# Performance work log

Hardware: AMD Instinct MI355X
Metric: run time of the kernel (lower is better)

The kernel has to match this reference:

```python
import jax, jax.numpy as jnp
import numpy as np

B, S, F, H, A = 256, 128, 512, 1024, 18


def setup_inputs() -> dict:
    key = jax.random.key(0)
    ks = jax.random.split(key, 16)
    u = lambda k, shape, fan: jax.random.uniform(k, shape, jnp.float32, -1.0, 1.0) / np.sqrt(fan)
    return {
        "obs": jax.random.normal(ks[0], (B, S, F), jnp.float32),
        "hx": jax.random.normal(ks[1], (B, H), jnp.float32),
        "cx": jax.random.normal(ks[2], (B, H), jnp.float32),
        "behaviour_acts": jax.random.randint(ks[3], (B, S, 1), 0, A),
        "W1": u(ks[4], (H, F), F), "b1": u(ks[5], (H,), F),
        "W_ih": u(ks[6], (4 * H, H), H), "b_ih": u(ks[7], (4 * H,), H),
        "W_hh": u(ks[8], (4 * H, H), H), "b_hh": u(ks[9], (4 * H,), H),
        "W_v": u(ks[10], (1, H), H), "b_v": u(ks[11], (1,), H),
        "W_l": u(ks[12], (A, H), H), "b_l": u(ks[13], (A,), H),
    }


def reference(obs, hx, cx, behaviour_acts, W1, b1, W_ih, b_ih, W_hh, b_hh, W_v, b_v, W_l, b_l):
    # MLP body: [B,S,F] -> [B,S,H]
    x = jax.nn.relu(jnp.einsum("bsf,hf->bsh", obs, W1) + b1)
    # precompute input-to-gate projection for all timesteps (one big GEMM)
    xg = jnp.einsum("bsh,gh->bsg", x, W_ih) + b_ih  # [B,S,4H]

    def step(carry, xg_t):
        h, c = carry
        gates = xg_t + h @ W_hh.T + b_hh  # [B,4H], gate order i,f,g,o (torch LSTMCell)
        i, f, g, o = jnp.split(gates, 4, axis=-1)
        c = jax.nn.sigmoid(f) * c + jax.nn.sigmoid(i) * jnp.tanh(g)
        h = jax.nn.sigmoid(o) * jnp.tanh(c)
        return (h, c), h

    _, hs = jax.lax.scan(step, (hx, cx), jnp.swapaxes(xg, 0, 1))
    output = jnp.swapaxes(hs, 0, 1)  # [B,S,H]

    value = output @ W_v.T + b_v  # [B,S,1]
    logits = output @ W_l.T + b_l  # [B,S,A]
    # torch Categorical(probs=softmax(logits)) => log-prob via log_softmax
    logp = jax.nn.log_softmax(logits, axis=-1)
    acts = behaviour_acts.reshape(logits.shape[0], logits.shape[1], 1)
    log_probs = jnp.take_along_axis(logp, acts, axis=-1)  # [B,S,1]
    entropy = -jnp.sum(jnp.exp(logp) * logp, axis=-1, keepdims=True)  # [B,S,1]
    return log_probs, entropy, value
```

## Files before the change

### kernel.cpp

```cpp
#include <hip/hip_runtime.h>

#define B_ 256
#define S_ 128
#define SP1 (S_+1)
#define F_ 512
#define H_ 1024
#define A_ 18
#define M_ (B_*S_)
#define G_ (4*H_)
#define CH_ 16
#define CR_ (B_*CH_)

typedef unsigned short u16;
typedef __attribute__((ext_vector_type(8))) _Float16 f16x8;
typedef __attribute__((ext_vector_type(4))) _Float16 f16x4;
typedef __attribute__((ext_vector_type(8))) short   s16x8;
typedef __attribute__((ext_vector_type(4))) float f32x4;
typedef __attribute__((ext_vector_type(4))) unsigned int u32x4;

__device__ __forceinline__ float bf2f(u16 u){
  union{unsigned int i; float f;} v; v.i=((unsigned int)u)<<16; return v.f;
}
__device__ __forceinline__ u16 f2bf(float f){
  unsigned int i=__float_as_uint(f);
  unsigned int r=(i+0x7fffu+((i>>16)&1u))>>16;
  return (u16)r;
}
__device__ __forceinline__ u16 f2h(float f){
  _Float16 h=(_Float16)f;
  union{_Float16 h; u16 u;} v; v.h=h; return v.u;
}
__device__ __forceinline__ float ldf(const void* p, size_t i, int m){
  return m ? ((const float*)p)[i] : bf2f(((const u16*)p)[i]);
}
__device__ __forceinline__ f16x8 load8_h(const void* base, size_t off, int m){
  f16x8 v;
  if(m==2) return *(const f16x8*)((const u16*)base + off);
  if(m==1){
    const float* f=(const float*)base + off;
    float4 a=*(const float4*)f; float4 b=*(const float4*)(f+4);
    v[0]=(_Float16)a.x; v[1]=(_Float16)a.y; v[2]=(_Float16)a.z; v[3]=(_Float16)a.w;
    v[4]=(_Float16)b.x; v[5]=(_Float16)b.y; v[6]=(_Float16)b.z; v[7]=(_Float16)b.w;
    return v;
  }
  s16x8 w=*(const s16x8*)((const u16*)base + off);
#pragma unroll
  for(int k=0;k<8;k++) v[k]=(_Float16)bf2f((u16)w[k]);
  return v;
}

__device__ __forceinline__ u32x4 load_c16(const void* p){
  u32x4 r;
  asm volatile("global_load_dwordx4 %0, %1, off sc0 sc1" : "=v"(r) : "v"(p));
  return r;
}
__device__ __forceinline__ void store_c2(u16* p, u16 v){
  unsigned int vv=v;
  asm volatile("global_store_short %0, %1, off sc0 sc1" :: "v"(p), "v"(vv) : "memory");
}
__device__ __forceinline__ int load_c4(const int* p){
  int r;
  asm volatile("global_load_dword %0, %1, off sc0 sc1" : "=v"(r) : "v"(p));
  return r;
}
__device__ __forceinline__ void store_c4(int* p, int v){
  asm volatile("global_store_dword %0, %1, off sc0 sc1" :: "v"(p), "v"(v) : "memory");
}

__device__ __forceinline__ void bar_flags32(int* flags, int target, int gi, int lane, int w){
  asm volatile("s_waitcnt vmcnt(0)" ::: "memory");
  __syncthreads();
  if(w==0){
    if(lane==0) store_c4(flags+gi, target);
    while(true){
      int v=load_c4(flags+(lane&31));
      asm volatile("s_waitcnt vmcnt(0)" ::: "memory");
      if(__all(v>=target)) break;
      __builtin_amdgcn_s_sleep(1);
    }
  }
  __syncthreads();
}

template<int ROWS, int MAP>
__device__ __forceinline__ void stage(const void* base, int mode, int lda, int k0,
                                      int rowoff, int t0, u16* lds, int tid){
  if(mode==2){
    constexpr int NI=(ROWS*8)/256;
    int wv=tid>>6, l=tid&63;
#pragma unroll
    for(int i=0;i<NI;i++){
      int s0=i*256+(wv<<6), s=s0+l;
      int r=s>>3, gc=(s&7)^(r&7);
      int p=rowoff+r, sr;
      if(MAP==0)      sr=p;
      else if(MAP==1) sr=(p&3)*H_+(p>>2);
      else            sr=(p>>4)*S_+t0+(p&15);
      const u16* src=(const u16*)base + (size_t)sr*lda + k0 + gc*8;
      u16* dst=lds + s0*8;
      __builtin_amdgcn_global_load_lds((const __attribute__((address_space(1))) unsigned int*)src,
                                       (__attribute__((address_space(3))) unsigned int*)dst,
                                       16, 0, 0);
    }
  } else {
#pragma unroll
    for(int s0=tid; s0<ROWS*8; s0+=256){
      int r=s0>>3, gc=s0&7, lc=gc^(r&7);
      int p=rowoff+r, sr;
      if(MAP==0)      sr=p;
      else if(MAP==1) sr=(p&3)*H_+(p>>2);
      else            sr=(p>>4)*S_+t0+(p&15);
      f16x8 v=load8_h(base, (size_t)sr*lda + k0 + gc*8, mode);
      *(f16x8*)(lds + r*64 + lc*8)=v;
    }
  }
}

__device__ __forceinline__ f16x8 frag_ld(const u16* lds, int r0, int kc, int lane){
  int r = r0 + (lane&15);
  int c = (kc + (lane>>4)) ^ (r&7);
  return *(const f16x8*)(lds + r*64 + c*8);
}

template<int AMAP, int BMAP, int OUTMODE>
__global__ __launch_bounds__(256,3) void gemm128(const void* A, const void* Bt, void* C,
    const float* __restrict__ biasf, const int* __restrict__ flag,
    int K, int lda, int ldb, int ldc, int t0, int amode, int bmode){
  int m=*flag;
  int am = amode<0 ? m : amode;
  int bm_ = bmode<0 ? m : bmode;
  __shared__ u16 As[128*64];
  __shared__ u16 Bs[128*64];
  int tid=threadIdx.x, lane=tid&63, w=tid>>6;
  int bm=blockIdx.y*128, bn=blockIdx.x*128;
  int wm=(w&1)*64, wn=(w>>1)*64;
  f32x4 acc[4][4];
#pragma unroll
  for(int i=0;i<4;i++)
#pragma unroll
    for(int j=0;j<4;j++) acc[i][j]=(f32x4)(0.f);
  for(int k0=0;k0<K;k0+=64){
    stage<128,AMAP>(A , am,  lda, k0, bm, t0, As, tid);
    stage<128,BMAP>(Bt, bm_, ldb, k0, bn, t0, Bs, tid);
    __syncthreads();
#pragma unroll
    for(int kk=0;kk<2;kk++){
      f16x8 af[4], bq[4];
#pragma unroll
      for(int i=0;i<4;i++) af[i]=frag_ld(As, wm+i*16, kk*4, lane);
#pragma unroll
      for(int j=0;j<4;j++) bq[j]=frag_ld(Bs, wn+j*16, kk*4, lane);
#pragma unroll
      for(int i=0;i<4;i++)
#pragma unroll
        for(int j=0;j<4;j++)
          acc[i][j]=__builtin_amdgcn_mfma_f32_16x16x32_f16(af[i],bq[j],acc[i][j],0,0,0);
    }
    __syncthreads();
  }
  int rl=lane>>4, cl=lane&15;
#pragma unroll
  for(int j=0;j<4;j++){
    int col=bn+wn+j*16+cl;
    float bb=biasf[col];
#pragma unroll
    for(int i=0;i<4;i++){
#pragma unroll
      for(int r=0;r<4;r++){
        int row=bm+wm+i*16+rl*4+r;
        float v=acc[i][j][r]+bb;
        if(OUTMODE==0){ v=fmaxf(v,0.f); ((u16*)C)[(size_t)row*ldc+col]=f2h(v); }
        else if(OUTMODE==2){ ((u16*)C)[(size_t)row*ldc+col]=f2h(v); }
        else { ((float*)C)[(size_t)row*ldc+col]=v; }
      }
    }
  }
}

__global__ __launch_bounds__(512,2) void lstm_persist(u16* __restrict__ hh,
        const u16* __restrict__ Whhp, const u16* __restrict__ xgp,
        float* __restrict__ cst, int* __restrict__ cntc, int tbase){
  __shared__ u16 As[16*2048];
  __shared__ float gs[32*132];
  int tid=threadIdx.x, lane=tid&63, w=tid>>6;
  int grp=blockIdx.x&7, ci=blockIdx.x>>3;
  int bm=grp*32, bn=ci*128;
  int* flags = cntc + grp*64;

  f16x8 bw[32];
#pragma unroll
  for(int t=0;t<32;t++){
    int p = bn + w*16 + (lane&15);
    int k = t*32 + (lane>>4)*8;
    bw[t]=*(const f16x8*)(Whhp + (size_t)p*H_ + k);
  }
#pragma unroll
  for(int t=0;t<32;t++) asm volatile("" : "+a"(bw[t]));

  int rl0=tid>>5, rl1=(tid+512)>>5, u0=tid&31;
  int gu=(bn>>2)+u0;
  float c0=cst[(size_t)(bm+rl0)*H_+gu];
  float c1=cst[(size_t)(bm+rl1)*H_+gu];

  for(int dt=0;dt<CH_;dt++){
    f16x4 xv0=*(const f16x4*)(xgp + ((size_t)(bm+rl0)*CH_+dt)*G_ + bn + u0*4);
    f16x4 xv1=*(const f16x4*)(xgp + ((size_t)(bm+rl1)*CH_+dt)*G_ + bn + u0*4);
    if(dt) bar_flags32(flags, tbase+dt, ci, lane, w);
    const u16* hbase = hh + (size_t)(tbase+dt)*H_;
    {
      u32x4 tmp[4];
#pragma unroll
      for(int i=0;i<4;i++){
        int s=tid+i*512, kt=s>>8, r=(s>>3)&31, gc=s&7;
        tmp[i]=*(const u32x4*)(hbase + (size_t)(bm+r)*(SP1*H_) + kt*64 + gc*8);
      }
#pragma unroll
      for(int i=0;i<4;i++){
        int s=tid+i*512, kt=s>>8, r=(s>>3)&31, gc=s&7, lc=gc^(r&7);
        *(u32x4*)(As + kt*2048 + r*64 + lc*8)=tmp[i];
      }
    }
    __syncthreads();
    u32x4 tmp2[4];
#pragma unroll
    for(int i=0;i<4;i++){
      int s=tid+(i+4)*512, kt=s>>8, r=(s>>3)&31, gc=s&7;
      tmp2[i]=*(const u32x4*)(hbase + (size_t)(bm+r)*(SP1*H_) + kt*64 + gc*8);
    }
    f32x4 acc0=(f32x4)(0.f), acc1=(f32x4)(0.f);
#pragma unroll
    for(int t=0;t<16;t++){
      int kt=t>>1, kk=t&1;
      f16x8 af0=frag_ld(As+kt*2048, 0,  kk*4, lane);
      f16x8 af1=frag_ld(As+kt*2048, 16, kk*4, lane);
      acc0=__builtin_amdgcn_mfma_f32_16x16x32_f16(af0,bw[t],acc0,0,0,0);
      acc1=__builtin_amdgcn_mfma_f32_16x16x32_f16(af1,bw[t],acc1,0,0,0);
    }
#pragma unroll
    for(int i=0;i<4;i++){
      int s=tid+(i+4)*512, kt=s>>8, r=(s>>3)&31, gc=s&7, lc=gc^(r&7);
      *(u32x4*)(As + kt*2048 + r*64 + lc*8)=tmp2[i];
    }
    __syncthreads();
#pragma unroll
    for(int t=16;t<32;t++){
      int kt=t>>1, kk=t&1;
      f16x8 af0=frag_ld(As+kt*2048, 0,  kk*4, lane);
      f16x8 af1=frag_ld(As+kt*2048, 16, kk*4, lane);
      acc0=__builtin_amdgcn_mfma_f32_16x16x32_f16(af0,bw[t],acc0,0,0,0);
      acc1=__builtin_amdgcn_mfma_f32_16x16x32_f16(af1,bw[t],acc1,0,0,0);
    }
#pragma unroll
    for(int r=0;r<4;r++){
      gs[(   (lane>>4)*4+r)*132 + w*16+(lane&15)]=acc0[r];
      gs[(16+(lane>>4)*4+r)*132 + w*16+(lane&15)]=acc1[r];
    }
    __syncthreads();
    {
      float4 gv=*(const float4*)&gs[rl0*132+u0*4];
      float ii=1.f/(1.f+__expf(-(gv.x+(float)xv0[0])));
      float ff=1.f/(1.f+__expf(-(gv.y+(float)xv0[1])));
      float gg=1.f-2.f/(__expf(2.f*(gv.z+(float)xv0[2]))+1.f);
      float oo=1.f/(1.f+__expf(-(gv.w+(float)xv0[3])));
      c0=ff*c0+ii*gg;
      float th=1.f-2.f/(__expf(2.f*c0)+1.f);
      store_c2(hh + ((size_t)(bm+rl0)*SP1 + tbase+dt+1)*H_ + gu, f2h(oo*th));
    }
    {
      float4 gv=*(const float4*)&gs[rl1*132+u0*4];
      float ii=1.f/(1.f+__expf(-(gv.x+(float)xv1[0])));
      float ff=1.f/(1.f+__expf(-(gv.y+(float)xv1[1])));
      float gg=1.f-2.f/(__expf(2.f*(gv.z+(float)xv1[2]))+1.f);
      float oo=1.f/(1.f+__expf(-(gv.w+(float)xv1[3])));
      c1=ff*c1+ii*gg;
      float th=1.f-2.f/(__expf(2.f*c1)+1.f);
      store_c2(hh + ((size_t)(bm+rl1)*SP1 + tbase+dt+1)*H_ + gu, f2h(oo*th));
    }
  }
  cst[(size_t)(bm+rl0)*H_+gu]=c0;
  cst[(size_t)(bm+rl1)*H_+gu]=c1;
}

__global__ __launch_bounds__(256,2) void lstm_step(u16* __restrict__ hh, int slotAbs, int dt,
        const void* __restrict__ Whh, const u16* __restrict__ xg,
        float* __restrict__ cst, const int* __restrict__ flag){
  int m=*flag;
  __shared__ u16 As[64*64];
  __shared__ u16 Bs[64*64];
  __shared__ float gs[64*64];
  int tid=threadIdx.x, lane=tid&63, w=tid>>6;
  int bm=blockIdx.y*64, bn=blockIdx.x*64;
  int wm=(w&1)*32, wn=(w>>1)*32;
  f32x4 acc[2][2];
#pragma unroll
  for(int i=0;i<2;i++)
#pragma unroll
    for(int j=0;j<2;j++) acc[i][j]=(f32x4)(0.f);
  for(int k0=0;k0<H_;k0+=64){
    stage<64,0>(hh + (size_t)slotAbs*H_, 2, SP1*H_, k0, bm, 0, As, tid);
    stage<64,1>(Whh,                     m, H_,     k0, bn, 0, Bs, tid);
    __syncthreads();
#pragma unroll
    for(int kk=0;kk<2;kk++){
      f16x8 af[2], bq[2];
#pragma unroll
      for(int i=0;i<2;i++) af[i]=frag_ld(As, wm+i*16, kk*4, lane);
#pragma unroll
      for(int j=0;j<2;j++) bq[j]=frag_ld(Bs, wn+j*16, kk*4, lane);
#pragma unroll
      for(int i=0;i<2;i++)
#pragma unroll
        for(int j=0;j<2;j++)
          acc[i][j]=__builtin_amdgcn_mfma_f32_16x16x32_f16(af[i],bq[j],acc[i][j],0,0,0);
    }
    __syncthreads();
  }
  int rl=lane>>4, cl=lane&15;
#pragma unroll
  for(int j=0;j<2;j++){
    int coll=wn+j*16+cl;
#pragma unroll
    for(int i=0;i<2;i++){
#pragma unroll
      for(int r=0;r<4;r++){
        int rowl=wm+i*16+rl*4+r;
        float xv=(float)((const _Float16*)xg)[((size_t)(bm+rowl)*CH_+dt)*G_ + bn+coll];
        gs[rowl*64+coll]=acc[i][j][r] + xv;
      }
    }
  }
  __syncthreads();
#pragma unroll
  for(int p=0;p<4;p++){
    int idx=p*256+tid;
    int rowl=idx>>4, u=idx&15;
    float4 gv = *(const float4*)&gs[rowl*64+u*4];
    float ii=1.f/(1.f+__expf(-gv.x));
    float ff=1.f/(1.f+__expf(-gv.y));
    float gg=1.f-2.f/(__expf(2.f*gv.z)+1.f);
    float oo=1.f/(1.f+__expf(-gv.w));
    int gb=bm+rowl;
    int gu=(bn>>2)+u;
    size_t ci=(size_t)gb*H_+gu;
    float cn=ff*cst[ci]+ii*gg;
    cst[ci]=cn;
    float th=1.f-2.f/(__expf(2.f*cn)+1.f);
    hh[((size_t)gb*SP1 + slotAbs+1)*H_ + gu]=f2h(oo*th);
  }
}

__global__ __launch_bounds__(256,2) void heads_full(const u16* __restrict__ hh,
      const void* __restrict__ Wl, const void* __restrict__ Wv,
      const float* __restrict__ blf, const int* __restrict__ acts,
      void* __restrict__ out, const int* __restrict__ flag){
  int m=*flag;
  int rg = blockIdx.x*4 + (threadIdx.x>>6);
  int lane = threadIdx.x & 63;
  int b=rg>>7, t=rg&(S_-1);
  const u16* h = hh + ((size_t)b*SP1 + t+1)*H_;
  u32x4 hv0=load_c16(h + lane*16);
  u32x4 hv1=load_c16(h + lane*16 + 8);
  f16x8 h0=__builtin_bit_cast(f16x8,hv0), h1=__builtin_bit_cast(f16x8,hv1);
  float hv[16];
#pragma unroll
  for(int k=0;k<8;k++){ hv[k]=(float)h0[k]; hv[8+k]=(float)h1[k]; }
  float dots[19];
#pragma unroll
  for(int j=0;j<19;j++){
    const void* wrow = (j<18) ? Wl : Wv;
    size_t roff = (j<18) ? (size_t)j*H_ : 0;
    float wv_[16];
    if(m){
      const float* f=(const float*)wrow + roff + lane*16;
      float4 a=*(const float4*)f, b2=*(const float4*)(f+4), c=*(const float4*)(f+8), d=*(const float4*)(f+12);
      wv_[0]=a.x;wv_[1]=a.y;wv_[2]=a.z;wv_[3]=a.w; wv_[4]=b2.x;wv_[5]=b2.y;wv_[6]=b2.z;wv_[7]=b2.w;
      wv_[8]=c.x;wv_[9]=c.y;wv_[10]=c.z;wv_[11]=c.w; wv_[12]=d.x;wv_[13]=d.y;wv_[14]=d.z;wv_[15]=d.w;
    } else {
      const u16* ub=(const u16*)wrow + roff + lane*16;
      s16x8 w0=*(const s16x8*)ub, w1=*(const s16x8*)(ub+8);
#pragma unroll
      for(int k=0;k<8;k++){ wv_[k]=bf2f((u16)w0[k]); wv_[8+k]=bf2f((u16)w1[k]); }
    }
    float d=0.f;
#pragma unroll
    for(int k=0;k<16;k++) d += hv[k]*wv_[k];
#pragma unroll
    for(int mm=1;mm<64;mm<<=1) d += __shfl_xor(d, mm, 64);
    dots[j]=d;
  }
  float lg[18];
#pragma unroll
  for(int j=0;j<18;j++) lg[j]=dots[j]+blf[j];
  float value=dots[18]+blf[18];
  float mx=lg[0];
#pragma unroll
  for(int j=1;j<18;j++) mx=fmaxf(mx,lg[j]);
  float se=0.f, s1=0.f;
#pragma unroll
  for(int j=0;j<18;j++){ float e=__expf(lg[j]-mx); se+=e; s1+=e*(lg[j]-mx); }
  float lse=__logf(se);
  int a=acts[rg];
  float la=0.f;
#pragma unroll
  for(int j=0;j<18;j++) la = (j==a) ? lg[j] : la;
  float lp=la-mx-lse;
  float ent=lse - s1/se;
  if(lane==0){
    if(m){
      ((float*)out)[rg]=lp; ((float*)out)[M_+rg]=ent; ((float*)out)[2*M_+rg]=value;
    } else {
      ((u16*)out)[rg]=f2bf(lp); ((u16*)out)[M_+rg]=f2bf(ent); ((u16*)out)[2*M_+rg]=f2bf(value);
    }
  }
}

__global__ void detect(const u16* __restrict__ obs_w, int* __restrict__ flag){
  __shared__ float red[256];
  float mx=0.f;
  for(int i=threadIdx.x;i<4096;i+=256) mx=fmaxf(mx,fabsf(bf2f(obs_w[i])));
  red[threadIdx.x]=mx; __syncthreads();
  for(int s=128;s>0;s>>=1){
    if(threadIdx.x<s) red[threadIdx.x]=fmaxf(red[threadIdx.x],red[threadIdx.x+s]);
    __syncthreads();
  }
  if(threadIdx.x==0) *flag=(red[0]>1e4f)?1:0;
}

__global__ void prep(const void* bih, const void* bhh, const void* b1, const void* bl, const void* bv,
                     const void* cx, const void* hx,
                     float* biasg, float* b1f, float* blf, float* cst, u16* hh,
                     int* cnt, const int* __restrict__ flag){
  int m=*flag;
  size_t i=(size_t)blockIdx.x*256+threadIdx.x;
  if(i<G_){ size_t rm=(i&3)*H_+(i>>2); biasg[i]=ldf(bih,rm,m)+ldf(bhh,rm,m); return; }
  i-=G_;
  if(i<H_){ b1f[i]=ldf(b1,i,m); return; }
  i-=H_;
  if(i<19){ blf[i]=(i<18)?ldf(bl,i,m):ldf(bv,0,m); return; }
  i-=19;
  if(i<512){ cnt[i]=0; return; }
  i-=512;
  if(i<(size_t)B_*H_){ cst[i]=ldf(cx,i,m); return; }
  i-=(size_t)B_*H_;
  if(i<(size_t)B_*H_){
    size_t b=i>>10, k=i&1023;
    hh[b*(SP1*H_) + k]=f2h(ldf(hx,i,m));
  }
}

__global__ void convw(const void* W1, const void* Wih, const void* Whh,
                      u16* W1h, u16* Wihp, u16* Whhp, const int* __restrict__ flag){
  int m=*flag;
  size_t i=((size_t)blockIdx.x*256+threadIdx.x)*8;
  const size_t n1=(size_t)H_*F_, n2=(size_t)G_*H_;
  if(i<n1){ *(f16x8*)(W1h+i)=load8_h(W1,i,m); return; }
  i-=n1;
  if(i<n2){ size_t p=i>>10, c=i&1023; size_t sr=(p&3)*H_+(p>>2);
            *(f16x8*)(Wihp+i)=load8_h(Wih, sr*H_+c, m); return; }
  i-=n2;
  if(i<n2){ size_t p=i>>10, c=i&1023; size_t sr=(p&3)*H_+(p>>2);
            *(f16x8*)(Whhp+i)=load8_h(Whh, sr*H_+c, m); return; }
}
__global__ void convobs(const void* obs, u16* obsh, const int* __restrict__ flag){
  int m=*flag;
  size_t i=((size_t)blockIdx.x*256+threadIdx.x)*8;
  if(i<(size_t)M_*F_) *(f16x8*)(obsh+i)=load8_h(obs,i,m);
}

extern "C" void kernel_launch(void* const* d_in, const int* in_sizes, int n_in,
                              void* d_out, int out_size, void* d_ws, size_t ws_size,
                              hipStream_t stream){
  const void* obs=d_in[0];
  const void* hx =d_in[1];
  const void* cx =d_in[2];
  const int* acts=(const int*)d_in[3];
  const void* W1 =d_in[4];
  const void* b1 =d_in[5];
  const void* Wih=d_in[6];
  const void* bih=d_in[7];
  const void* Whh=d_in[8];
  const void* bhh=d_in[9];
  const void* Wv =d_in[10];
  const void* bv =d_in[11];
  const void* Wl =d_in[12];
  const void* bl =d_in[13];

  char* w=(char*)d_ws;
  auto alloc=[&](size_t n){ char* p=w; w+=((n+255)&~(size_t)255); return p; };
  int*   flag =(int*)alloc(4);
  int*   cnt  =(int*)alloc(512*4);
  float* biasg=(float*)alloc((size_t)G_*4);
  float* b1f  =(float*)alloc((size_t)H_*4);
  float* blf  =(float*)alloc(32*4);
  float* cst  =(float*)alloc((size_t)B_*H_*4);
  u16*   hh   =(u16*)alloc((size_t)B_*SP1*H_*2);
  u16*   xc   =(u16*)alloc((size_t)CR_*H_*2);
  u16*   xg   =(u16*)alloc((size_t)CR_*G_*2);
  size_t nW=((size_t)H_*F_ + 2*(size_t)G_*H_)*2 + 768;
  bool pathW = ((size_t)(w-(char*)d_ws) + nW) <= ws_size;
  u16 *W1h=0,*Wihp=0,*Whhp=0;
  if(pathW){ W1h=(u16*)alloc((size_t)H_*F_*2); Wihp=(u16*)alloc((size_t)G_*H_*2); Whhp=(u16*)alloc((size_t)G_*H_*2); }
  size_t nXC=(size_t)M_*H_*2 + 256;
  bool pathXC = pathW && (((size_t)(w-(char*)d_ws) + nXC) <= ws_size);
  u16* xcf=0; if(pathXC) xcf=(u16*)alloc((size_t)M_*H_*2);
  size_t nO=(size_t)M_*F_*2 + 256;
  bool pathO = pathXC && (((size_t)(w-(char*)d_ws) + nO) <= ws_size);
  u16* obsh=0; if(pathO) obsh=(u16*)alloc((size_t)M_*F_*2);

  detect<<<1,256,0,stream>>>((const u16*)obs, flag);
  {
    int total=G_+H_+19+512+B_*H_+B_*H_;
    prep<<<(total+255)/256,256,0,stream>>>(bih,bhh,b1,bl,bv,cx,hx, biasg,b1f,blf,cst,hh,cnt, flag);
  }
  if(pathW){
    size_t n=((size_t)H_*F_+2*(size_t)G_*H_)/8;
    convw<<<(int)((n+255)/256),256,0,stream>>>(W1,Wih,Whh, W1h,Wihp,Whhp, flag);
  }
  if(pathO){
    size_t n=(size_t)M_*F_/8;
    convobs<<<(int)((n+255)/256),256,0,stream>>>(obs, obsh, flag);
  }
  if(pathXC){
    gemm128<0,0,0><<<dim3(H_/128, M_/128),256,0,stream>>>(
        pathO?(const void*)obsh:obs, pathW?(const void*)W1h:W1, xcf, b1f, flag,
        F_, F_, F_, H_, 0, pathO?2:-1, pathW?2:-1);
  }

  const int NC=S_/CH_;
  for(int c=0;c<NC;c++){
    int t0=c*CH_;
    if(!pathXC){
      gemm128<2,0,0><<<dim3(H_/128, CR_/128),256,0,stream>>>(
          obs, pathW?(const void*)W1h:W1, xc, b1f, flag, F_, F_, F_, H_, t0, -1, pathW?2:-1);
    }
    if(pathXC)
      gemm128<2,0,2><<<dim3(G_/128, CR_/128),256,0,stream>>>(
          xcf, Wihp, xg, biasg, flag, H_, H_, H_, G_, t0, 2, 2);
    else if(pathW)
      gemm128<0,0,2><<<dim3(G_/128, CR_/128),256,0,stream>>>(
          xc, Wihp, xg, biasg, flag, H_, H_, H_, G_, 0, 2, 2);
    else
      gemm128<0,1,2><<<dim3(G_/128, CR_/128),256,0,stream>>>(
          xc, Wih, xg, biasg, flag, H_, H_, H_, G_, 0, 2, -1);

    if(pathW)
      lstm_persist<<<256,512,0,stream>>>(hh, Whhp, xg, cst, cnt, t0);
    else
      for(int dt=0;dt<CH_;dt++)
        lstm_step<<<dim3(G_/64, B_/64),256,0,stream>>>(hh, t0+dt, dt, Whh, xg, cst, flag);
  }

  heads_full<<<dim3(M_/4),256,0,stream>>>(hh, Wl, Wv, blf, acts, d_out, flag);
}
```

Before: 1.238 ms.

## Compute policy/value heads with an MFMA GEMM kernel over packed f16 head weights

```diff
diff --git a/kernel.cpp b/kernel.cpp
--- a/kernel.cpp
+++ b/kernel.cpp
@@ -49,11 +49,6 @@
   return v;
 }
 
-__device__ __forceinline__ u32x4 load_c16(const void* p){
-  u32x4 r;
-  asm volatile("global_load_dwordx4 %0, %1, off sc0 sc1" : "=v"(r) : "v"(p));
-  return r;
-}
 __device__ __forceinline__ void store_c2(u16* p, u16 v){
   unsigned int vv=v;
   asm volatile("global_store_short %0, %1, off sc0 sc1" :: "v"(p), "v"(vv) : "memory");
@@ -349,6 +344,78 @@
   }
 }
 
+__global__ __launch_bounds__(512,1) void heads_gemm(const u16* __restrict__ hh,
+      const u16* __restrict__ WH, const float* __restrict__ blf,
+      const int* __restrict__ acts, void* __restrict__ out, const int* __restrict__ flag){
+  int m=*flag;
+  __shared__ u16 Bs[16*2048];
+  __shared__ u16 As[128*64];
+  __shared__ float gs[128*36];
+  int tid=threadIdx.x, lane=tid&63, w=tid>>6;
+  int bm=blockIdx.x*128;
+#pragma unroll
+  for(int i=0;i<8;i++){
+    int s=tid+i*512;
+    int kt=s>>8, r=(s>>3)&31, gc=s&7, lc=gc^(r&7);
+    *(f16x8*)(Bs+kt*2048+r*64+lc*8) = *(const f16x8*)(WH + (size_t)r*H_ + kt*64 + gc*8);
+  }
+  f32x4 acc0=(f32x4)(0.f), acc1=(f32x4)(0.f);
+  for(int kt=0;kt<16;kt++){
+#pragma unroll
+    for(int i=0;i<2;i++){
+      int s0=i*512+(w<<6), s=s0+lane;
+      int r=s>>3, gc=(s&7)^(r&7);
+      int rg=bm+r;
+      const u16* src=hh + ((size_t)(rg>>7)*SP1 + (rg&127)+1)*H_ + kt*64 + gc*8;
+      u16* dst=As + s0*8;
+      __builtin_amdgcn_global_load_lds((const __attribute__((address_space(1))) unsigned int*)src,
+                                       (__attribute__((address_space(3))) unsigned int*)dst,
+                                       16, 0, 0);
+    }
+    __syncthreads();
+#pragma unroll
+    for(int kk=0;kk<2;kk++){
+      f16x8 af=frag_ld(As, w*16, kk*4, lane);
+      f16x8 b0=frag_ld(Bs+kt*2048, 0,  kk*4, lane);
+      f16x8 b1=frag_ld(Bs+kt*2048, 16, kk*4, lane);
+      acc0=__builtin_amdgcn_mfma_f32_16x16x32_f16(af,b0,acc0,0,0,0);
+      acc1=__builtin_amdgcn_mfma_f32_16x16x32_f16(af,b1,acc1,0,0,0);
+    }
+    __syncthreads();
+  }
+#pragma unroll
+  for(int r=0;r<4;r++){
+    gs[(w*16+(lane>>4)*4+r)*36 + (lane&15)]      = acc0[r];
+    gs[(w*16+(lane>>4)*4+r)*36 + 16 + (lane&15)] = acc1[r];
+  }
+  __syncthreads();
+  if(tid<128){
+    int rg=bm+tid;
+    float lg[18];
+#pragma unroll
+    for(int j=0;j<18;j++) lg[j]=gs[tid*36+j]+blf[j];
+    float value=gs[tid*36+18]+blf[18];
+    float mx=lg[0];
+#pragma unroll
+    for(int j=1;j<18;j++) mx=fmaxf(mx,lg[j]);
+    float se=0.f, s1=0.f;
+#pragma unroll
+    for(int j=0;j<18;j++){ float e=__expf(lg[j]-mx); se+=e; s1+=e*(lg[j]-mx); }
+    float lse=__logf(se);
+    int a=acts[rg];
+    float la=0.f;
+#pragma unroll
+    for(int j=0;j<18;j++) la = (j==a) ? lg[j] : la;
+    float lp=la-mx-lse;
+    float ent=lse - s1/se;
+    if(m){
+      ((float*)out)[rg]=lp; ((float*)out)[M_+rg]=ent; ((float*)out)[2*M_+rg]=value;
+    } else {
+      ((u16*)out)[rg]=f2bf(lp); ((u16*)out)[M_+rg]=f2bf(ent); ((u16*)out)[2*M_+rg]=f2bf(value);
+    }
+  }
+}
+
 __global__ __launch_bounds__(256,2) void heads_full(const u16* __restrict__ hh,
       const void* __restrict__ Wl, const void* __restrict__ Wv,
       const float* __restrict__ blf, const int* __restrict__ acts,
@@ -358,9 +425,7 @@
   int lane = threadIdx.x & 63;
   int b=rg>>7, t=rg&(S_-1);
   const u16* h = hh + ((size_t)b*SP1 + t+1)*H_;
-  u32x4 hv0=load_c16(h + lane*16);
-  u32x4 hv1=load_c16(h + lane*16 + 8);
-  f16x8 h0=__builtin_bit_cast(f16x8,hv0), h1=__builtin_bit_cast(f16x8,hv1);
+  f16x8 h0=*(const f16x8*)(h + lane*16), h1=*(const f16x8*)(h + lane*16 + 8);
   float hv[16];
 #pragma unroll
   for(int k=0;k<8;k++){ hv[k]=(float)h0[k]; hv[8+k]=(float)h1[k]; }
@@ -449,10 +514,12 @@
 }
 
 __global__ void convw(const void* W1, const void* Wih, const void* Whh,
-                      u16* W1h, u16* Wihp, u16* Whhp, const int* __restrict__ flag){
+                      const void* Wl, const void* Wv,
+                      u16* W1h, u16* Wihp, u16* Whhp, u16* WH,
+                      const int* __restrict__ flag){
   int m=*flag;
   size_t i=((size_t)blockIdx.x*256+threadIdx.x)*8;
-  const size_t n1=(size_t)H_*F_, n2=(size_t)G_*H_;
+  const size_t n1=(size_t)H_*F_, n2=(size_t)G_*H_, n3=(size_t)32*H_;
   if(i<n1){ *(f16x8*)(W1h+i)=load8_h(W1,i,m); return; }
   i-=n1;
   if(i<n2){ size_t p=i>>10, c=i&1023; size_t sr=(p&3)*H_+(p>>2);
@@ -460,6 +527,15 @@
   i-=n2;
   if(i<n2){ size_t p=i>>10, c=i&1023; size_t sr=(p&3)*H_+(p>>2);
             *(f16x8*)(Whhp+i)=load8_h(Whh, sr*H_+c, m); return; }
+  i-=n2;
+  if(i<n3){
+    size_t j=i>>10, c=i&1023;
+    f16x8 v;
+    if(j<18)      v=load8_h(Wl, j*H_+c, m);
+    else if(j==18) v=load8_h(Wv, c, m);
+    else{ for(int k=0;k<8;k++) v[k]=(_Float16)0.f; }
+    *(f16x8*)(WH+i)=v;
+  }
 }
 __global__ void convobs(const void* obs, u16* obsh, const int* __restrict__ flag){
   int m=*flag;
@@ -496,10 +572,11 @@
   u16*   hh   =(u16*)alloc((size_t)B_*SP1*H_*2);
   u16*   xc   =(u16*)alloc((size_t)CR_*H_*2);
   u16*   xg   =(u16*)alloc((size_t)CR_*G_*2);
-  size_t nW=((size_t)H_*F_ + 2*(size_t)G_*H_)*2 + 768;
+  size_t nW=((size_t)H_*F_ + 2*(size_t)G_*H_ + 32*(size_t)H_)*2 + 1024;
   bool pathW = ((size_t)(w-(char*)d_ws) + nW) <= ws_size;
-  u16 *W1h=0,*Wihp=0,*Whhp=0;
-  if(pathW){ W1h=(u16*)alloc((size_t)H_*F_*2); Wihp=(u16*)alloc((size_t)G_*H_*2); Whhp=(u16*)alloc((size_t)G_*H_*2); }
+  u16 *W1h=0,*Wihp=0,*Whhp=0,*WH=0;
+  if(pathW){ W1h=(u16*)alloc((size_t)H_*F_*2); Wihp=(u16*)alloc((size_t)G_*H_*2);
+             Whhp=(u16*)alloc((size_t)G_*H_*2); WH=(u16*)alloc((size_t)32*H_*2); }
   size_t nXC=(size_t)M_*H_*2 + 256;
   bool pathXC = pathW && (((size_t)(w-(char*)d_ws) + nXC) <= ws_size);
   u16* xcf=0; if(pathXC) xcf=(u16*)alloc((size_t)M_*H_*2);
@@ -513,8 +590,8 @@
     prep<<<(total+255)/256,256,0,stream>>>(bih,bhh,b1,bl,bv,cx,hx, biasg,b1f,blf,cst,hh,cnt, flag);
   }
   if(pathW){
-    size_t n=((size_t)H_*F_+2*(size_t)G_*H_)/8;
-    convw<<<(int)((n+255)/256),256,0,stream>>>(W1,Wih,Whh, W1h,Wihp,Whhp, flag);
+    size_t n=((size_t)H_*F_+2*(size_t)G_*H_+32*(size_t)H_)/8;
+    convw<<<(int)((n+255)/256),256,0,stream>>>(W1,Wih,Whh,Wl,Wv, W1h,Wihp,Whhp,WH, flag);
   }
   if(pathO){
     size_t n=(size_t)M_*F_/8;
@@ -550,5 +627,8 @@
         lstm_step<<<dim3(G_/64, B_/64),256,0,stream>>>(hh, t0+dt, dt, Whh, xg, cst, flag);
   }
 
-  heads_full<<<dim3(M_/4),256,0,stream>>>(hh, Wl, Wv, blf, acts, d_out, flag);
-}
+  if(pathW)
+    heads_gemm<<<dim3(M_/128),512,0,stream>>>(hh, WH, blf, acts, d_out, flag);
+  else
+    heads_full<<<dim3(M_/4),256,0,stream>>>(hh, Wl, Wv, blf, acts, d_out, flag);
+}
```

After: 1.107 ms. 1.12x faster.
